# Optimization experiments

Hardware: AMD Instinct MI355X
Metric: run time of the kernel (lower is better)

Reference implementation:

```python
import jax, jax.numpy as jnp
import numpy as np
import math

B, C, N, L = 32, 128, 2048, 1
H, DK, APT = 8, 16, 10
EPS = 1e-5


def conv1x1(x, W, b):
    # 1x1 Conv2d on [B, C, N, L]
    return jnp.einsum('oc,bcnl->bonl', W, x) + b[None, :, None, None]


def layer_norm_12(x):
    # normalize over dims (1, 2) as in the custom LayerNorm (no affine)
    mean = x.mean(axis=(1, 2), keepdims=True)
    var = x.var(axis=(1, 2), keepdims=True)
    return (x - mean) / jnp.sqrt(var + EPS)


def setup_inputs() -> dict:
    key = jax.random.key(0)
    ks = jax.random.split(key, 10)
    s = 0.05  # small-scale init for numerical stability
    inp = {
        'input': jax.random.normal(ks[0], (B, C, N, L), jnp.float32),
        'Wq': jax.random.normal(ks[1], (C, C), jnp.float32) * s,
        'bq': jnp.zeros((C,), jnp.float32),
        'Wv': jax.random.normal(ks[2], (C, C), jnp.float32) * s,
        'bv': jnp.zeros((C,), jnp.float32),
        'Wc': jax.random.normal(ks[3], (C, C), jnp.float32) * s,
        'bc': jnp.zeros((C,), jnp.float32),
        'memory': jax.random.normal(ks[4], (H, L, N, DK), jnp.float32) * s,
        'sa_weight': jnp.ones((C, N, L), jnp.float32),
        'sa_bias': jnp.zeros((C, N, L), jnp.float32),
        'nodevec1': jax.random.normal(ks[5], (N, APT), jnp.float32),
        'nodevec2': jax.random.normal(ks[6], (APT, N), jnp.float32),
        'Wg1': jax.random.normal(ks[7], (C, C), jnp.float32) * s,
        'bg1': jnp.zeros((C,), jnp.float32),
        'Wg2': jax.random.normal(ks[8], (C, C), jnp.float32) * s,
        'bg2': jnp.zeros((C,), jnp.float32),
        'Wg3': jax.random.normal(ks[9], (C, C), jnp.float32) * s,
        'bg3': jnp.zeros((C,), jnp.float32),
    }
    return inp


def reference(input, Wq, bq, Wv, bv, Wc, bc, memory, sa_weight, sa_bias,
              nodevec1, nodevec2, Wg1, bg1, Wg2, bg2, Wg3, bg3):
    scale = math.sqrt(DK)

    def split_heads(t):  # [B,C,N,L] -> [B,H,L,N,DK]
        return t.reshape(B, H, DK, N, L).transpose(0, 1, 4, 3, 2)

    # SpatialAttention (Conv = 1x1 conv + relu; dropout off in eval)
    q = jax.nn.relu(conv1x1(input, Wq, bq))
    v = jax.nn.relu(conv1x1(input, Wv, bv))
    query = jax.nn.softmax(split_heads(q) / scale, axis=-1)     # [B,H,L,N,DK]
    value = split_heads(v)                                       # [B,H,L,N,DK]
    key = jax.nn.softmax(memory / scale, axis=-1)                # [H,L,N,DK]
    Aapt = jax.nn.softmax(jax.nn.relu(nodevec1 @ nodevec2), axis=-1)  # [N,N]

    kv = jnp.einsum('hlnx,bhlny->bhlxy', key, value)             # [B,H,L,DK,DK]
    attn_qkv = jnp.einsum('bhlnx,bhlxy->bhlny', query, kv)       # [B,H,L,N,DK]
    attn_dyn = jnp.einsum('nm,bhlnc->bhlnc', Aapt, value)        # row-sum scaling
    x = attn_qkv + attn_dyn

    # merge heads back to [B,C,N,L] and apply concat conv (Conv = conv+relu)
    x = x.transpose(0, 1, 4, 3, 2).reshape(B, C, N, L)
    x = jax.nn.relu(conv1x1(x, Wc, bc))
    x = x * sa_weight[None] + sa_bias[None] + x                  # affine branch

    # Encoder wrap
    x = x + input
    x = layer_norm_12(x)
    g = conv1x1(x, Wg1, bg1) * jax.nn.sigmoid(conv1x1(x, Wg2, bg2))
    g = conv1x1(g, Wg3, bg3)                                     # GLU
    x = g + x
    x = x * sa_weight[None] + sa_bias[None] + x
    x = layer_norm_12(x)
    return x
```

## Files before the change

kernel.cpp:

```cpp
#include <hip/hip_runtime.h>
#include <math.h>

#define DI __device__ __forceinline__

typedef short bf16x8 __attribute__((ext_vector_type(8)));
typedef float f32x4 __attribute__((ext_vector_type(4)));

constexpr int BB = 32, CC = 128, NN = 2048, HH = 8;
constexpr float EPSf = 1e-5f;
constexpr float RCN = 1.0f / (CC * (float)NN);

#define MFMA(a,b,c) __builtin_amdgcn_mfma_f32_16x16x32_bf16(a,b,c,0,0,0)

DI unsigned short f2b(float f){
    union { float f; unsigned u; } v; v.f = f;
    return (unsigned short)((v.u + 0x7FFFu + ((v.u >> 16) & 1u)) >> 16);
}
DI float b2f(unsigned short h){
    union { unsigned u; float f; } v; v.u = ((unsigned)h) << 16;
    return v.f;
}
DI float sigm(float x){ return 1.0f / (1.0f + __expf(-x)); }

__global__ __launch_bounds__(256) void k_keysm(const float* __restrict__ mem,
                                               unsigned short* __restrict__ ksT)
{
    const int row = blockIdx.x * 256 + threadIdx.x;
    const int h = row >> 11, n = row & 2047;
    const float* p = mem + (size_t)row * 16;
    float v[16];
    f32x4 t0 = *(const f32x4*)(p);
    f32x4 t1 = *(const f32x4*)(p + 4);
    f32x4 t2 = *(const f32x4*)(p + 8);
    f32x4 t3 = *(const f32x4*)(p + 12);
#pragma unroll
    for (int j = 0; j < 4; j++) { v[j] = t0[j]; v[4+j] = t1[j]; v[8+j] = t2[j]; v[12+j] = t3[j]; }
    float mx = v[0];
#pragma unroll
    for (int x = 1; x < 16; x++) mx = fmaxf(mx, v[x]);
    float s = 0.f;
#pragma unroll
    for (int x = 0; x < 16; x++) { v[x] = __expf((v[x] - mx) * 0.25f); s += v[x]; }
    const float is = 1.0f / s;
#pragma unroll
    for (int x = 0; x < 16; x++)
        ksT[((size_t)(h * 16 + x)) * NN + n] = f2b(v[x] * is);
}

__global__ __launch_bounds__(256,2) void k_qv(
    const float* __restrict__ in, const float* __restrict__ Wq, const float* __restrict__ bq,
    const float* __restrict__ Wv, const float* __restrict__ bv,
    unsigned short* __restrict__ qT, unsigned short* __restrict__ vT)
{
    __shared__ unsigned short Wa[128*136];
    __shared__ unsigned short Wb[128*136];
    const int b = blockIdx.x >> 4;
    const int n0 = (blockIdx.x & 15) * 128;
    const int tid = threadIdx.x;
#pragma unroll
    for (int r = 0; r < 16; r++) {
        const int i4 = r * 256 + tid, o = i4 >> 5, cq = i4 & 31;
        f32x4 w1 = *(const f32x4*)&Wq[o*128 + cq*4];
        f32x4 w2 = *(const f32x4*)&Wv[o*128 + cq*4];
        ushort4 p1, p2;
        p1.x=f2b(w1[0]); p1.y=f2b(w1[1]); p1.z=f2b(w1[2]); p1.w=f2b(w1[3]);
        p2.x=f2b(w2[0]); p2.y=f2b(w2[1]); p2.z=f2b(w2[2]); p2.w=f2b(w2[3]);
        *(ushort4*)&Wa[o*136 + cq*4] = p1;
        *(ushort4*)&Wb[o*136 + cq*4] = p2;
    }
    __syncthreads();
    const int l = tid & 63, wid = tid >> 6;
    const int wo = wid & 1, wn = wid >> 1;
    const int lr = l & 15, lg = l >> 4;
    f32x4 accq[4][4], accv[4][4];
    const f32x4 z = {0.f,0.f,0.f,0.f};
#pragma unroll
    for (int i = 0; i < 4; i++)
#pragma unroll
        for (int j = 0; j < 4; j++) { accq[i][j] = z; accv[i][j] = z; }
    const float* inb = in + (size_t)b * CC * NN;
#pragma unroll
    for (int ks = 0; ks < 4; ks++) {
        const int cb = ks*32 + lg*8;
        bf16x8 aq[4], av[4];
#pragma unroll
        for (int mf = 0; mf < 4; mf++) {
            const int o = wo*64 + mf*16 + lr;
            aq[mf] = *(const bf16x8*)&Wa[o*136 + cb];
            av[mf] = *(const bf16x8*)&Wb[o*136 + cb];
        }
        bf16x8 bx[4];
#pragma unroll
        for (int nf = 0; nf < 4; nf++) {
            const int n = n0 + wn*64 + nf*16 + lr;
            union { bf16x8 v; unsigned short u[8]; } t;
#pragma unroll
            for (int j = 0; j < 8; j++) t.u[j] = f2b(inb[(size_t)(cb + j) * NN + n]);
            bx[nf] = t.v;
        }
#pragma unroll
        for (int mf = 0; mf < 4; mf++)
#pragma unroll
            for (int nf = 0; nf < 4; nf++) {
                accq[mf][nf] = MFMA(aq[mf], bx[nf], accq[mf][nf]);
                accv[mf][nf] = MFMA(av[mf], bx[nf], accv[mf][nf]);
            }
    }
#pragma unroll
    for (int mf = 0; mf < 4; mf++) {
        const int ob = wo*64 + mf*16 + lg*4;
        const f32x4 bq4 = *(const f32x4*)&bq[ob];
        const f32x4 bv4 = *(const f32x4*)&bv[ob];
#pragma unroll
        for (int nf = 0; nf < 4; nf++) {
            const int n = n0 + wn*64 + nf*16 + lr;
            const size_t yo = ((size_t)b * NN + n) * CC + ob;
            f32x4 aq_ = accq[mf][nf], av_ = accv[mf][nf];
            ushort4 pq, pv;
            pq.x = f2b(fmaxf(aq_[0]+bq4[0],0.f)); pq.y = f2b(fmaxf(aq_[1]+bq4[1],0.f));
            pq.z = f2b(fmaxf(aq_[2]+bq4[2],0.f)); pq.w = f2b(fmaxf(aq_[3]+bq4[3],0.f));
            pv.x = f2b(fmaxf(av_[0]+bv4[0],0.f)); pv.y = f2b(fmaxf(av_[1]+bv4[1],0.f));
            pv.z = f2b(fmaxf(av_[2]+bv4[2],0.f)); pv.w = f2b(fmaxf(av_[3]+bv4[3],0.f));
            *(ushort4*)&qT[yo] = pq;
            *(ushort4*)&vT[yo] = pv;
        }
    }
}

__global__ __launch_bounds__(256) void k_kv(const unsigned short* __restrict__ ksT,
                                            const unsigned short* __restrict__ vT,
                                            float* __restrict__ kvb)
{
    __shared__ unsigned short vt[4 * 16 * 520];
    const int bh = blockIdx.x;
    const int b = bh >> 3, h = bh & 7;
    const int tid = threadIdx.x, l = tid & 63, wid = tid >> 6;
    const int n0 = wid * 512;
    unsigned short* vtw = vt + wid * (16 * 520);
    const unsigned short* vb = vT + ((size_t)b * NN + n0) * CC + h * 16;
#pragma unroll
    for (int r = 0; r < 8; r++) {
        const int nl = r * 64 + l;
        ushort4 p0 = *(const ushort4*)&vb[(size_t)nl * CC + 0];
        ushort4 p1 = *(const ushort4*)&vb[(size_t)nl * CC + 4];
        ushort4 p2 = *(const ushort4*)&vb[(size_t)nl * CC + 8];
        ushort4 p3 = *(const ushort4*)&vb[(size_t)nl * CC + 12];
        vtw[ 0*520+nl]=p0.x; vtw[ 1*520+nl]=p0.y; vtw[ 2*520+nl]=p0.z; vtw[ 3*520+nl]=p0.w;
        vtw[ 4*520+nl]=p1.x; vtw[ 5*520+nl]=p1.y; vtw[ 6*520+nl]=p1.z; vtw[ 7*520+nl]=p1.w;
        vtw[ 8*520+nl]=p2.x; vtw[ 9*520+nl]=p2.y; vtw[10*520+nl]=p2.z; vtw[11*520+nl]=p2.w;
        vtw[12*520+nl]=p3.x; vtw[13*520+nl]=p3.y; vtw[14*520+nl]=p3.z; vtw[15*520+nl]=p3.w;
    }
    const int lr = l & 15, lg = l >> 4;
    const unsigned short* ka = ksT + (size_t)h * 16 * NN;
    f32x4 acc = {0.f,0.f,0.f,0.f};
#pragma unroll
    for (int kk = 0; kk < 16; kk++) {
        bf16x8 af = *(const bf16x8*)&ka[(size_t)lr * NN + n0 + kk*32 + lg*8];
        bf16x8 bf = *(const bf16x8*)&vtw[lr * 520 + kk*32 + lg*8];
        acc = MFMA(af, bf, acc);
    }
    float* kp = kvb + ((size_t)(b * 8 + h)) * 256;
#pragma unroll
    for (int r = 0; r < 4; r++)
        atomicAdd(&kp[(lg*4 + r) * 16 + lr], acc[r]);
}

__global__ __launch_bounds__(256) void k_attn(unsigned short* __restrict__ qT,
                                              const unsigned short* __restrict__ vT,
                                              const float* __restrict__ kvb)
{
    __shared__ float kvl[8 * 260];
    const int b = blockIdx.x >> 6, nb = blockIdx.x & 63;
    const int tid = threadIdx.x;
    {
        const float* kp = kvb + (size_t)b * 2048 + (tid >> 5) * 256 + (tid & 31) * 8;
        f32x4 v0 = *(const f32x4*)kp;
        f32x4 v1 = *(const f32x4*)(kp + 4);
        float* dst = &kvl[(tid >> 5) * 260 + (tid & 31) * 8];
        *(f32x4*)dst = v0; *(f32x4*)(dst + 4) = v1;
    }
    __syncthreads();
    const int h = tid & 7, nl = tid >> 3;
    const int n = nb * 32 + nl;
    unsigned short* qp = qT + ((size_t)b * NN + n) * CC + h * 16;
    const unsigned short* vp = vT + ((size_t)b * NN + n) * CC + h * 16;
    float q[16];
    {
        uint4 u0 = *(const uint4*)qp, u1 = *(const uint4*)(qp + 8);
        unsigned uu[8] = {u0.x,u0.y,u0.z,u0.w,u1.x,u1.y,u1.z,u1.w};
#pragma unroll
        for (int j = 0; j < 8; j++) {
            q[2*j]   = b2f((unsigned short)(uu[j] & 0xffffu));
            q[2*j+1] = b2f((unsigned short)(uu[j] >> 16));
        }
    }
    float mx = q[0];
#pragma unroll
    for (int x = 1; x < 16; x++) mx = fmaxf(mx, q[x]);
    float p[16]; float s = 0.f;
#pragma unroll
    for (int x = 0; x < 16; x++) { p[x] = __expf((q[x] - mx) * 0.25f); s += p[x]; }
    const float is = 1.0f / s;
    const float* kh = &kvl[h * 260];
    float r[16];
#pragma unroll
    for (int y = 0; y < 16; y++) r[y] = 0.f;
#pragma unroll
    for (int x = 0; x < 16; x++) {
        const float px = p[x];
#pragma unroll
        for (int y = 0; y < 16; y++) r[y] = fmaf(px, kh[x * 16 + y], r[y]);
    }
    unsigned w[8];
    {
        uint4 u0 = *(const uint4*)vp, u1 = *(const uint4*)(vp + 8);
        unsigned uu[8] = {u0.x,u0.y,u0.z,u0.w,u1.x,u1.y,u1.z,u1.w};
#pragma unroll
        for (int j = 0; j < 8; j++) {
            float o0 = r[2*j]   * is + b2f((unsigned short)(uu[j] & 0xffffu));
            float o1 = r[2*j+1] * is + b2f((unsigned short)(uu[j] >> 16));
            w[j] = (unsigned)f2b(o0) | ((unsigned)f2b(o1) << 16);
        }
    }
    uint4 o0; o0.x=w[0]; o0.y=w[1]; o0.z=w[2]; o0.w=w[3];
    uint4 o1; o1.x=w[4]; o1.y=w[5]; o1.z=w[6]; o1.w=w[7];
    *(uint4*)qp = o0; *(uint4*)(qp + 8) = o1;
}

template<int EPI>
__global__ __launch_bounds__(256,2) void k_gemmC(
    const unsigned short* __restrict__ act, const float* __restrict__ W,
    const float* __restrict__ bias, const float* __restrict__ saw,
    const float* __restrict__ sab, const float* __restrict__ in0f,
    const unsigned short* __restrict__ e0b, const float* __restrict__ statsIn,
    float* __restrict__ statsOut, unsigned short* __restrict__ Y)
{
    __shared__ unsigned short Wl[128*136];
    __shared__ float red[8];
    const int b = blockIdx.x >> 4;
    const int n0 = (blockIdx.x & 15) * 128;
    const int tid = threadIdx.x;
    float mean = 0.f, inv = 0.f;
    if (EPI == 1) {
        mean = statsIn[2*b] * RCN;
        const float var = statsIn[2*b+1] * RCN - mean * mean;
        inv = rsqrtf(var + EPSf);
    }
#pragma unroll
    for (int r = 0; r < 16; r++) {
        const int i4 = r * 256 + tid, o = i4 >> 5, cq = i4 & 31;
        f32x4 w1 = *(const f32x4*)&W[o*128 + cq*4];
        ushort4 p1;
        p1.x=f2b(w1[0]); p1.y=f2b(w1[1]); p1.z=f2b(w1[2]); p1.w=f2b(w1[3]);
        *(ushort4*)&Wl[o*136 + cq*4] = p1;
    }
    __syncthreads();
    const int l = tid & 63, wid = tid >> 6;
    const int wo = wid & 1, wn = wid >> 1;
    const int lr = l & 15, lg = l >> 4;
    f32x4 acc[4][4];
    const f32x4 z = {0.f,0.f,0.f,0.f};
#pragma unroll
    for (int i = 0; i < 4; i++)
#pragma unroll
        for (int j = 0; j < 4; j++) acc[i][j] = z;
    const unsigned short* ab = act + (size_t)b * NN * CC;
#pragma unroll
    for (int ks = 0; ks < 4; ks++) {
        const int cb = ks*32 + lg*8;
        bf16x8 af[4];
#pragma unroll
        for (int mf = 0; mf < 4; mf++)
            af[mf] = *(const bf16x8*)&Wl[(wo*64 + mf*16 + lr)*136 + cb];
        bf16x8 bx[4];
#pragma unroll
        for (int nf = 0; nf < 4; nf++)
            bx[nf] = *(const bf16x8*)&ab[(size_t)(n0 + wn*64 + nf*16 + lr) * CC + cb];
#pragma unroll
        for (int mf = 0; mf < 4; mf++)
#pragma unroll
            for (int nf = 0; nf < 4; nf++)
                acc[mf][nf] = MFMA(af[mf], bx[nf], acc[mf][nf]);
    }
    float sum = 0.f, ssq = 0.f;
#pragma unroll
    for (int mf = 0; mf < 4; mf++) {
        const int ob = wo*64 + mf*16 + lg*4;
        const f32x4 b4 = *(const f32x4*)&bias[ob];
#pragma unroll
        for (int nf = 0; nf < 4; nf++) {
            const int n = n0 + wn*64 + nf*16 + lr;
            const size_t yo = ((size_t)b * NN + n) * CC + ob;
            f32x4 a = acc[mf][nf];
            ushort4 eu;
            if (EPI == 1) eu = *(const ushort4*)&e0b[yo];
            ushort4 pk;
            float ys[4];
#pragma unroll
            for (int r = 0; r < 4; r++) {
                const int o = ob + r;
                float t;
                if (EPI == 0) {
                    t = fmaxf(a[r] + b4[r], 0.f);
                } else {
                    const unsigned short ev = (r==0)?eu.x:(r==1)?eu.y:(r==2)?eu.z:eu.w;
                    t = a[r] + b4[r] + (b2f(ev) - mean) * inv;
                }
                const float sw = saw[(size_t)o * NN + n];
                const float sb = sab[(size_t)o * NN + n];
                float y = t * sw + sb + t;
                if (EPI == 0) y += in0f[((size_t)b * CC + o) * NN + n];
                sum += y; ssq += y * y;
                ys[r] = y;
            }
            pk.x = f2b(ys[0]); pk.y = f2b(ys[1]); pk.z = f2b(ys[2]); pk.w = f2b(ys[3]);
            *(ushort4*)&Y[yo] = pk;
        }
    }
#pragma unroll
    for (int off = 32; off > 0; off >>= 1) {
        sum += __shfl_down(sum, off);
        ssq += __shfl_down(ssq, off);
    }
    if ((tid & 63) == 0) { red[wid*2] = sum; red[wid*2+1] = ssq; }
    __syncthreads();
    if (tid == 0) {
        float s = red[0]+red[2]+red[4]+red[6];
        float q = red[1]+red[3]+red[5]+red[7];
        atomicAdd(&statsOut[2*b], s);
        atomicAdd(&statsOut[2*b+1], q);
    }
}

__global__ __launch_bounds__(256,2) void k_glu12(
    const unsigned short* __restrict__ y1, const float* __restrict__ W1,
    const float* __restrict__ b1, const float* __restrict__ W2,
    const float* __restrict__ b2, const float* __restrict__ stats1,
    unsigned short* __restrict__ G)
{
    __shared__ unsigned short Wl1[128*136];
    __shared__ unsigned short Wl2[128*136];
    __shared__ float cs[256];
    const int b = blockIdx.x >> 4;
    const int n0 = (blockIdx.x & 15) * 128;
    const int tid = threadIdx.x;
    const float mean = stats1[2*b] * RCN;
    const float var = stats1[2*b+1] * RCN - mean * mean;
    const float inv = rsqrtf(var + EPSf);
#pragma unroll
    for (int r = 0; r < 16; r++) {
        const int i4 = r * 256 + tid, o = i4 >> 5, cq = i4 & 31;
        f32x4 w1 = *(const f32x4*)&W1[o*128 + cq*4];
        f32x4 w2 = *(const f32x4*)&W2[o*128 + cq*4];
        ushort4 p1, p2;
        p1.x=f2b(w1[0]); p1.y=f2b(w1[1]); p1.z=f2b(w1[2]); p1.w=f2b(w1[3]);
        p2.x=f2b(w2[0]); p2.y=f2b(w2[1]); p2.z=f2b(w2[2]); p2.w=f2b(w2[3]);
        *(ushort4*)&Wl1[o*136 + cq*4] = p1;
        *(ushort4*)&Wl2[o*136 + cq*4] = p2;
    }
    {
        const int o = tid >> 1, hf = tid & 1;
        float s1 = 0.f, s2 = 0.f;
#pragma unroll
        for (int j4 = 0; j4 < 16; j4++) {
            f32x4 a = *(const f32x4*)&W1[o*128 + hf*64 + j4*4];
            f32x4 c = *(const f32x4*)&W2[o*128 + hf*64 + j4*4];
            s1 += a[0]+a[1]+a[2]+a[3];
            s2 += c[0]+c[1]+c[2]+c[3];
        }
        s1 += __shfl_xor(s1, 1);
        s2 += __shfl_xor(s2, 1);
        cs[o]       = b1[o] - mean * inv * s1;
        cs[128 + o] = b2[o] - mean * inv * s2;
    }
    __syncthreads();
    const int l = tid & 63, wid = tid >> 6;
    const int wo = wid & 1, wn = wid >> 1;
    const int lr = l & 15, lg = l >> 4;
    f32x4 acc1[4][4], acc2[4][4];
    const f32x4 z = {0.f,0.f,0.f,0.f};
#pragma unroll
    for (int i = 0; i < 4; i++)
#pragma unroll
        for (int j = 0; j < 4; j++) { acc1[i][j] = z; acc2[i][j] = z; }
    const unsigned short* ab = y1 + (size_t)b * NN * CC;
#pragma unroll
    for (int ks = 0; ks < 4; ks++) {
        const int cb = ks*32 + lg*8;
        bf16x8 a1[4], a2[4];
#pragma unroll
        for (int mf = 0; mf < 4; mf++) {
            const int o = wo*64 + mf*16 + lr;
            a1[mf] = *(const bf16x8*)&Wl1[o*136 + cb];
            a2[mf] = *(const bf16x8*)&Wl2[o*136 + cb];
        }
        bf16x8 bx[4];
#pragma unroll
        for (int nf = 0; nf < 4; nf++)
            bx[nf] = *(const bf16x8*)&ab[(size_t)(n0 + wn*64 + nf*16 + lr) * CC + cb];
#pragma unroll
        for (int mf = 0; mf < 4; mf++)
#pragma unroll
            for (int nf = 0; nf < 4; nf++) {
                acc1[mf][nf] = MFMA(a1[mf], bx[nf], acc1[mf][nf]);
                acc2[mf][nf] = MFMA(a2[mf], bx[nf], acc2[mf][nf]);
            }
    }
#pragma unroll
    for (int mf = 0; mf < 4; mf++) {
        const int ob = wo*64 + mf*16 + lg*4;
        const f32x4 c1 = *(const f32x4*)&cs[ob];
        const f32x4 c2 = *(const f32x4*)&cs[128 + ob];
#pragma unroll
        for (int nf = 0; nf < 4; nf++) {
            const int n = n0 + wn*64 + nf*16 + lr;
            const size_t yo = ((size_t)b * NN + n) * CC + ob;
            ushort4 pk;
            float g1, g2;
            g1 = acc1[mf][nf][0]*inv + c1[0]; g2 = acc2[mf][nf][0]*inv + c2[0];
            pk.x = f2b(g1 * sigm(g2));
            g1 = acc1[mf][nf][1]*inv + c1[1]; g2 = acc2[mf][nf][1]*inv + c2[1];
            pk.y = f2b(g1 * sigm(g2));
            g1 = acc1[mf][nf][2]*inv + c1[2]; g2 = acc2[mf][nf][2]*inv + c2[2];
            pk.z = f2b(g1 * sigm(g2));
            g1 = acc1[mf][nf][3]*inv + c1[3]; g2 = acc2[mf][nf][3]*inv + c2[3];
            pk.w = f2b(g1 * sigm(g2));
            *(ushort4*)&G[yo] = pk;
        }
    }
}

__global__ __launch_bounds__(256) void k_lnfin(const unsigned short* __restrict__ x2,
                                               const float* __restrict__ st,
                                               float* __restrict__ out)
{
    __shared__ unsigned short ts[64*136];
    const int b = blockIdx.x >> 5, n0 = (blockIdx.x & 31) * 64;
    const float mean = st[2*b] * RCN;
    const float var = st[2*b+1] * RCN - mean * mean;
    const float inv = rsqrtf(var + EPSf);
    const int tid = threadIdx.x;
    {
        const int n = tid >> 2, qd = tid & 3;
        const unsigned short* src = x2 + ((size_t)b * NN + n0 + n) * CC + qd * 32;
        uint4 a0 = *(const uint4*)(src);
        uint4 a1 = *(const uint4*)(src + 8);
        uint4 a2 = *(const uint4*)(src + 16);
        uint4 a3 = *(const uint4*)(src + 24);
        unsigned short* d = &ts[n*136 + qd*32];
        *(uint4*)(d) = a0; *(uint4*)(d+8) = a1; *(uint4*)(d+16) = a2; *(uint4*)(d+24) = a3;
    }
    __syncthreads();
    {
        const int c = tid >> 1, nh = tid & 1;
        float* op = out + ((size_t)b * CC + c) * NN + n0 + nh * 32;
        f32x4 buf;
#pragma unroll
        for (int j = 0; j < 32; j++) {
            buf[j & 3] = (b2f(ts[(nh*32 + j)*136 + c]) - mean) * inv;
            if ((j & 3) == 3) *(f32x4*)(op + (j - 3)) = buf;
        }
    }
}

extern "C" void kernel_launch(void* const* d_in, const int* in_sizes, int n_in,
                              void* d_out, int out_size, void* d_ws, size_t ws_size,
                              hipStream_t stream)
{
    const float* input = (const float*)d_in[0];
    const float* Wq  = (const float*)d_in[1];
    const float* bq  = (const float*)d_in[2];
    const float* Wv  = (const float*)d_in[3];
    const float* bv  = (const float*)d_in[4];
    const float* Wc  = (const float*)d_in[5];
    const float* bc  = (const float*)d_in[6];
    const float* mem = (const float*)d_in[7];
    const float* saw = (const float*)d_in[8];
    const float* sab = (const float*)d_in[9];
    const float* Wg1 = (const float*)d_in[12];
    const float* bg1 = (const float*)d_in[13];
    const float* Wg2 = (const float*)d_in[14];
    const float* bg2 = (const float*)d_in[15];
    const float* Wg3 = (const float*)d_in[16];
    const float* bg3 = (const float*)d_in[17];
    float* out = (float*)d_out;

    unsigned char* wsb = (unsigned char*)d_ws;
    unsigned short* qT  = (unsigned short*)(wsb);
    unsigned short* vT  = (unsigned short*)(wsb + 16777216);
    unsigned short* ksT = (unsigned short*)(wsb + 2*16777216);
    float* kvb   = (float*)(wsb + 2*16777216 + 524288);
    float* stats = (float*)(wsb + 2*16777216 + 524288 + 262144);

    hipMemsetAsync(kvb, 0, 262144 + 512, stream);

    k_keysm<<<64,   256, 0, stream>>>(mem, ksT);
    k_qv   <<<512,  256, 0, stream>>>(input, Wq, bq, Wv, bv, qT, vT);
    k_kv   <<<256,  256, 0, stream>>>(ksT, vT, kvb);
    k_attn <<<2048, 256, 0, stream>>>(qT, vT, kvb);
    k_gemmC<0><<<512, 256, 0, stream>>>(qT, Wc, bc, saw, sab, input,
                                        nullptr, nullptr, stats, vT);
    k_glu12<<<512, 256, 0, stream>>>(vT, Wg1, bg1, Wg2, bg2, stats, qT);
    k_gemmC<1><<<512, 256, 0, stream>>>(qT, Wg3, bg3, saw, sab, nullptr,
                                        vT, stats, stats + 64, vT);
    k_lnfin<<<1024, 256, 0, stream>>>(vT, stats + 64, out);
}
```

Before: 143.8 us.

## Fuse attention with concat conv and GLU stages, pre-convert weights once

Adds a prep kernel that converts all six weight matrices to bf16 once and precomputes row sums, so GEMM kernels read bf16 weights straight from global memory instead of converting them into shared memory per block. The attention step is fused with the Wc conv through a shared-memory tile. The three GLU convolutions are fused into one kernel that keeps the intermediate gate tile in LDS. Atomic accumulation for kv and the layer-norm statistics is replaced by per-block partial sums that later kernels reduce, which also removes the memset. The final transpose uses a padded 32-bit shared layout. Trade-offs: higher LDS use per block and repeated partial-sum reductions in each consumer kernel.

Result: faster. 135.4 us (-5.9%).

```diff
diff --git a/kernel.cpp b/kernel.cpp
--- a/kernel.cpp
+++ b/kernel.cpp
@@ -1,4 +1,5 @@
 #include <hip/hip_runtime.h>
+#include <hip/hip_bf16.h>
 #include <math.h>
 
 #define DI __device__ __forceinline__
@@ -6,21 +7,49 @@
 typedef short bf16x8 __attribute__((ext_vector_type(8)));
 typedef float f32x4 __attribute__((ext_vector_type(4)));
 
-constexpr int BB = 32, CC = 128, NN = 2048, HH = 8;
+constexpr int BB = 32, CC = 128, NN = 2048;
 constexpr float EPSf = 1e-5f;
 constexpr float RCN = 1.0f / (CC * (float)NN);
 
 #define MFMA(a,b,c) __builtin_amdgcn_mfma_f32_16x16x32_bf16(a,b,c,0,0,0)
 
 DI unsigned short f2b(float f){
-    union { float f; unsigned u; } v; v.f = f;
-    return (unsigned short)((v.u + 0x7FFFu + ((v.u >> 16) & 1u)) >> 16);
+    union { __hip_bfloat16 h; unsigned short u; } v;
+    v.h = __float2bfloat16(f);
+    return v.u;
 }
 DI float b2f(unsigned short h){
     union { unsigned u; float f; } v; v.u = ((unsigned)h) << 16;
     return v.f;
 }
 DI float sigm(float x){ return 1.0f / (1.0f + __expf(-x)); }
+
+__global__ __launch_bounds__(256) void k_prep(
+    const float* __restrict__ Wq, const float* __restrict__ Wv,
+    const float* __restrict__ Wc, const float* __restrict__ Wg1,
+    const float* __restrict__ Wg2, const float* __restrict__ Wg3,
+    unsigned short* __restrict__ Wb, float* __restrict__ rs)
+{
+    const int tid = threadIdx.x;
+    if (blockIdx.x < 96) {
+        const int i = blockIdx.x * 256 + tid;
+        const int m = i >> 12, q = i & 4095;
+        const float* src = (m==0)?Wq:(m==1)?Wv:(m==2)?Wc:(m==3)?Wg1:(m==4)?Wg2:Wg3;
+        f32x4 w = *(const f32x4*)&src[q * 4];
+        ushort4 p; p.x=f2b(w[0]); p.y=f2b(w[1]); p.z=f2b(w[2]); p.w=f2b(w[3]);
+        *(ushort4*)&Wb[(size_t)m * 16384 + q * 4] = p;
+    } else {
+        const float* src = (tid < 128) ? Wg1 : Wg2;
+        const int o = tid & 127;
+        float s = 0.f;
+#pragma unroll
+        for (int j = 0; j < 32; j++) {
+            f32x4 a = *(const f32x4*)&src[o * 128 + j * 4];
+            s += a[0] + a[1] + a[2] + a[3];
+        }
+        rs[tid] = s;
+    }
+}
 
 __global__ __launch_bounds__(256) void k_keysm(const float* __restrict__ mem,
                                                unsigned short* __restrict__ ksT)
@@ -34,7 +63,7 @@
     f32x4 t2 = *(const f32x4*)(p + 8);
     f32x4 t3 = *(const f32x4*)(p + 12);
 #pragma unroll
-    for (int j = 0; j < 4; j++) { v[j] = t0[j]; v[4+j] = t1[j]; v[8+j] = t2[j]; v[12+j] = t3[j]; }
+    for (int j = 0; j < 4; j++) { v[j]=t0[j]; v[4+j]=t1[j]; v[8+j]=t2[j]; v[12+j]=t3[j]; }
     float mx = v[0];
 #pragma unroll
     for (int x = 1; x < 16; x++) mx = fmaxf(mx, v[x]);
@@ -48,30 +77,14 @@
 }
 
 __global__ __launch_bounds__(256,2) void k_qv(
-    const float* __restrict__ in, const float* __restrict__ Wq, const float* __restrict__ bq,
-    const float* __restrict__ Wv, const float* __restrict__ bv,
-    unsigned short* __restrict__ qT, unsigned short* __restrict__ vT)
-{
-    __shared__ unsigned short Wa[128*136];
-    __shared__ unsigned short Wb[128*136];
-    const int b = blockIdx.x >> 4;
-    const int n0 = (blockIdx.x & 15) * 128;
-    const int tid = threadIdx.x;
-#pragma unroll
-    for (int r = 0; r < 16; r++) {
-        const int i4 = r * 256 + tid, o = i4 >> 5, cq = i4 & 31;
-        f32x4 w1 = *(const f32x4*)&Wq[o*128 + cq*4];
-        f32x4 w2 = *(const f32x4*)&Wv[o*128 + cq*4];
-        ushort4 p1, p2;
-        p1.x=f2b(w1[0]); p1.y=f2b(w1[1]); p1.z=f2b(w1[2]); p1.w=f2b(w1[3]);
-        p2.x=f2b(w2[0]); p2.y=f2b(w2[1]); p2.z=f2b(w2[2]); p2.w=f2b(w2[3]);
-        *(ushort4*)&Wa[o*136 + cq*4] = p1;
-        *(ushort4*)&Wb[o*136 + cq*4] = p2;
-    }
-    __syncthreads();
-    const int l = tid & 63, wid = tid >> 6;
-    const int wo = wid & 1, wn = wid >> 1;
-    const int lr = l & 15, lg = l >> 4;
+    const float* __restrict__ in, const unsigned short* __restrict__ WqB,
+    const unsigned short* __restrict__ WvB, const float* __restrict__ bq,
+    const float* __restrict__ bv, unsigned short* __restrict__ qT,
+    unsigned short* __restrict__ vT)
+{
+    const int b = blockIdx.x >> 4, n0 = (blockIdx.x & 15) * 128;
+    const int tid = threadIdx.x, l = tid & 63, wid = tid >> 6;
+    const int wo = wid & 1, wn = wid >> 1, lr = l & 15, lg = l >> 4;
     f32x4 accq[4][4], accv[4][4];
     const f32x4 z = {0.f,0.f,0.f,0.f};
 #pragma unroll
@@ -81,13 +94,13 @@
     const float* inb = in + (size_t)b * CC * NN;
 #pragma unroll
     for (int ks = 0; ks < 4; ks++) {
-        const int cb = ks*32 + lg*8;
+        const int cb = ks * 32 + lg * 8;
         bf16x8 aq[4], av[4];
 #pragma unroll
         for (int mf = 0; mf < 4; mf++) {
             const int o = wo*64 + mf*16 + lr;
-            aq[mf] = *(const bf16x8*)&Wa[o*136 + cb];
-            av[mf] = *(const bf16x8*)&Wb[o*136 + cb];
+            aq[mf] = *(const bf16x8*)&WqB[o * 128 + cb];
+            av[mf] = *(const bf16x8*)&WvB[o * 128 + cb];
         }
         bf16x8 bx[4];
 #pragma unroll
@@ -132,8 +145,8 @@
                                             float* __restrict__ kvb)
 {
     __shared__ unsigned short vt[4 * 16 * 520];
-    const int bh = blockIdx.x;
-    const int b = bh >> 3, h = bh & 7;
+    __shared__ float red[1024];
+    const int b = blockIdx.x >> 3, h = blockIdx.x & 7;
     const int tid = threadIdx.x, l = tid & 63, wid = tid >> 6;
     const int n0 = wid * 512;
     unsigned short* vtw = vt + wid * (16 * 520);
@@ -159,18 +172,27 @@
         bf16x8 bf = *(const bf16x8*)&vtw[lr * 520 + kk*32 + lg*8];
         acc = MFMA(af, bf, acc);
     }
-    float* kp = kvb + ((size_t)(b * 8 + h)) * 256;
 #pragma unroll
     for (int r = 0; r < 4; r++)
-        atomicAdd(&kp[(lg*4 + r) * 16 + lr], acc[r]);
-}
-
-__global__ __launch_bounds__(256) void k_attn(unsigned short* __restrict__ qT,
-                                              const unsigned short* __restrict__ vT,
-                                              const float* __restrict__ kvb)
+        red[wid * 256 + (lg*4 + r) * 16 + lr] = acc[r];
+    __syncthreads();
+    {
+        const float s = red[tid] + red[256 + tid] + red[512 + tid] + red[768 + tid];
+        kvb[((size_t)(b * 8 + h)) * 256 + tid] = s;
+    }
+}
+
+__global__ __launch_bounds__(256,2) void k_attnC(
+    const unsigned short* __restrict__ qT, unsigned short* __restrict__ vT,
+    const float* __restrict__ kvb, const unsigned short* __restrict__ WcB,
+    const float* __restrict__ bc, const float* __restrict__ saw,
+    const float* __restrict__ sab, const float* __restrict__ in0f,
+    float* __restrict__ part1)
 {
     __shared__ float kvl[8 * 260];
-    const int b = blockIdx.x >> 6, nb = blockIdx.x & 63;
+    __shared__ unsigned short xc[128 * 136];
+    __shared__ float red[8];
+    const int b = blockIdx.x >> 4, n0 = (blockIdx.x & 15) * 128;
     const int tid = threadIdx.x;
     {
         const float* kp = kvb + (size_t)b * 2048 + (tid >> 5) * 256 + (tid & 31) * 8;
@@ -180,102 +202,73 @@
         *(f32x4*)dst = v0; *(f32x4*)(dst + 4) = v1;
     }
     __syncthreads();
-    const int h = tid & 7, nl = tid >> 3;
-    const int n = nb * 32 + nl;
-    unsigned short* qp = qT + ((size_t)b * NN + n) * CC + h * 16;
-    const unsigned short* vp = vT + ((size_t)b * NN + n) * CC + h * 16;
-    float q[16];
-    {
-        uint4 u0 = *(const uint4*)qp, u1 = *(const uint4*)(qp + 8);
-        unsigned uu[8] = {u0.x,u0.y,u0.z,u0.w,u1.x,u1.y,u1.z,u1.w};
-#pragma unroll
-        for (int j = 0; j < 8; j++) {
-            q[2*j]   = b2f((unsigned short)(uu[j] & 0xffffu));
-            q[2*j+1] = b2f((unsigned short)(uu[j] >> 16));
-        }
-    }
-    float mx = q[0];
-#pragma unroll
-    for (int x = 1; x < 16; x++) mx = fmaxf(mx, q[x]);
-    float p[16]; float s = 0.f;
-#pragma unroll
-    for (int x = 0; x < 16; x++) { p[x] = __expf((q[x] - mx) * 0.25f); s += p[x]; }
-    const float is = 1.0f / s;
-    const float* kh = &kvl[h * 260];
-    float r[16];
-#pragma unroll
-    for (int y = 0; y < 16; y++) r[y] = 0.f;
-#pragma unroll
-    for (int x = 0; x < 16; x++) {
-        const float px = p[x];
-#pragma unroll
-        for (int y = 0; y < 16; y++) r[y] = fmaf(px, kh[x * 16 + y], r[y]);
-    }
-    unsigned w[8];
-    {
-        uint4 u0 = *(const uint4*)vp, u1 = *(const uint4*)(vp + 8);
-        unsigned uu[8] = {u0.x,u0.y,u0.z,u0.w,u1.x,u1.y,u1.z,u1.w};
-#pragma unroll
-        for (int j = 0; j < 8; j++) {
-            float o0 = r[2*j]   * is + b2f((unsigned short)(uu[j] & 0xffffu));
-            float o1 = r[2*j+1] * is + b2f((unsigned short)(uu[j] >> 16));
-            w[j] = (unsigned)f2b(o0) | ((unsigned)f2b(o1) << 16);
-        }
-    }
-    uint4 o0; o0.x=w[0]; o0.y=w[1]; o0.z=w[2]; o0.w=w[3];
-    uint4 o1; o1.x=w[4]; o1.y=w[5]; o1.z=w[6]; o1.w=w[7];
-    *(uint4*)qp = o0; *(uint4*)(qp + 8) = o1;
-}
-
-template<int EPI>
-__global__ __launch_bounds__(256,2) void k_gemmC(
-    const unsigned short* __restrict__ act, const float* __restrict__ W,
-    const float* __restrict__ bias, const float* __restrict__ saw,
-    const float* __restrict__ sab, const float* __restrict__ in0f,
-    const unsigned short* __restrict__ e0b, const float* __restrict__ statsIn,
-    float* __restrict__ statsOut, unsigned short* __restrict__ Y)
-{
-    __shared__ unsigned short Wl[128*136];
-    __shared__ float red[8];
-    const int b = blockIdx.x >> 4;
-    const int n0 = (blockIdx.x & 15) * 128;
-    const int tid = threadIdx.x;
-    float mean = 0.f, inv = 0.f;
-    if (EPI == 1) {
-        mean = statsIn[2*b] * RCN;
-        const float var = statsIn[2*b+1] * RCN - mean * mean;
-        inv = rsqrtf(var + EPSf);
-    }
-#pragma unroll
-    for (int r = 0; r < 16; r++) {
-        const int i4 = r * 256 + tid, o = i4 >> 5, cq = i4 & 31;
-        f32x4 w1 = *(const f32x4*)&W[o*128 + cq*4];
-        ushort4 p1;
-        p1.x=f2b(w1[0]); p1.y=f2b(w1[1]); p1.z=f2b(w1[2]); p1.w=f2b(w1[3]);
-        *(ushort4*)&Wl[o*136 + cq*4] = p1;
+#pragma unroll
+    for (int it = 0; it < 4; it++) {
+        const int idx = it * 256 + tid;
+        const int nl = idx >> 3, h = idx & 7;
+        const size_t base = ((size_t)b * NN + n0 + nl) * CC + h * 16;
+        const unsigned short* qp = qT + base;
+        const unsigned short* vp = vT + base;
+        float q[16];
+        {
+            uint4 u0 = *(const uint4*)qp, u1 = *(const uint4*)(qp + 8);
+            unsigned uu[8] = {u0.x,u0.y,u0.z,u0.w,u1.x,u1.y,u1.z,u1.w};
+#pragma unroll
+            for (int j = 0; j < 8; j++) {
+                q[2*j]   = b2f((unsigned short)(uu[j] & 0xffffu));
+                q[2*j+1] = b2f((unsigned short)(uu[j] >> 16));
+            }
+        }
+        float mx = q[0];
+#pragma unroll
+        for (int x = 1; x < 16; x++) mx = fmaxf(mx, q[x]);
+        float p[16]; float s = 0.f;
+#pragma unroll
+        for (int x = 0; x < 16; x++) { p[x] = __expf((q[x] - mx) * 0.25f); s += p[x]; }
+        const float is = 1.0f / s;
+        const float* kh = &kvl[h * 260];
+        float r[16];
+#pragma unroll
+        for (int y = 0; y < 16; y++) r[y] = 0.f;
+#pragma unroll
+        for (int x = 0; x < 16; x++) {
+            const float px = p[x];
+#pragma unroll
+            for (int y = 0; y < 16; y++) r[y] = fmaf(px, kh[x * 16 + y], r[y]);
+        }
+        uint4 w0 = *(const uint4*)vp, w1 = *(const uint4*)(vp + 8);
+        unsigned vv[8] = {w0.x,w0.y,w0.z,w0.w,w1.x,w1.y,w1.z,w1.w};
+        unsigned short* xp = &xc[nl * 136 + h * 16];
+#pragma unroll
+        for (int j2 = 0; j2 < 4; j2++) {
+            ushort4 pk;
+            pk.x = f2b(r[4*j2+0]*is + b2f((unsigned short)(vv[2*j2]   & 0xffffu)));
+            pk.y = f2b(r[4*j2+1]*is + b2f((unsigned short)(vv[2*j2]   >> 16)));
+            pk.z = f2b(r[4*j2+2]*is + b2f((unsigned short)(vv[2*j2+1] & 0xffffu)));
+            pk.w = f2b(r[4*j2+3]*is + b2f((unsigned short)(vv[2*j2+1] >> 16)));
+            *(ushort4*)&xp[j2 * 4] = pk;
+        }
     }
     __syncthreads();
     const int l = tid & 63, wid = tid >> 6;
-    const int wo = wid & 1, wn = wid >> 1;
-    const int lr = l & 15, lg = l >> 4;
+    const int wo = wid & 1, wn = wid >> 1, lr = l & 15, lg = l >> 4;
     f32x4 acc[4][4];
     const f32x4 z = {0.f,0.f,0.f,0.f};
 #pragma unroll
     for (int i = 0; i < 4; i++)
 #pragma unroll
         for (int j = 0; j < 4; j++) acc[i][j] = z;
-    const unsigned short* ab = act + (size_t)b * NN * CC;
 #pragma unroll
     for (int ks = 0; ks < 4; ks++) {
-        const int cb = ks*32 + lg*8;
+        const int cb = ks * 32 + lg * 8;
         bf16x8 af[4];
 #pragma unroll
         for (int mf = 0; mf < 4; mf++)
-            af[mf] = *(const bf16x8*)&Wl[(wo*64 + mf*16 + lr)*136 + cb];
+            af[mf] = *(const bf16x8*)&WcB[(wo*64 + mf*16 + lr) * 128 + cb];
         bf16x8 bx[4];
 #pragma unroll
         for (int nf = 0; nf < 4; nf++)
-            bx[nf] = *(const bf16x8*)&ab[(size_t)(n0 + wn*64 + nf*16 + lr) * CC + cb];
+            bx[nf] = *(const bf16x8*)&xc[(wn*64 + nf*16 + lr) * 136 + cb];
 #pragma unroll
         for (int mf = 0; mf < 4; mf++)
 #pragma unroll
@@ -286,35 +279,26 @@
 #pragma unroll
     for (int mf = 0; mf < 4; mf++) {
         const int ob = wo*64 + mf*16 + lg*4;
-        const f32x4 b4 = *(const f32x4*)&bias[ob];
+        const f32x4 b4 = *(const f32x4*)&bc[ob];
 #pragma unroll
         for (int nf = 0; nf < 4; nf++) {
             const int n = n0 + wn*64 + nf*16 + lr;
             const size_t yo = ((size_t)b * NN + n) * CC + ob;
             f32x4 a = acc[mf][nf];
-            ushort4 eu;
-            if (EPI == 1) eu = *(const ushort4*)&e0b[yo];
-            ushort4 pk;
             float ys[4];
 #pragma unroll
             for (int r = 0; r < 4; r++) {
                 const int o = ob + r;
-                float t;
-                if (EPI == 0) {
-                    t = fmaxf(a[r] + b4[r], 0.f);
-                } else {
-                    const unsigned short ev = (r==0)?eu.x:(r==1)?eu.y:(r==2)?eu.z:eu.w;
-                    t = a[r] + b4[r] + (b2f(ev) - mean) * inv;
-                }
+                const float t = fmaxf(a[r] + b4[r], 0.f);
                 const float sw = saw[(size_t)o * NN + n];
                 const float sb = sab[(size_t)o * NN + n];
-                float y = t * sw + sb + t;
-                if (EPI == 0) y += in0f[((size_t)b * CC + o) * NN + n];
+                float y = t * sw + sb + t + in0f[((size_t)b * CC + o) * NN + n];
                 sum += y; ssq += y * y;
                 ys[r] = y;
             }
+            ushort4 pk;
             pk.x = f2b(ys[0]); pk.y = f2b(ys[1]); pk.z = f2b(ys[2]); pk.w = f2b(ys[3]);
-            *(ushort4*)&Y[yo] = pk;
+            *(ushort4*)&vT[yo] = pk;
         }
     }
 #pragma unroll
@@ -325,121 +309,180 @@
     if ((tid & 63) == 0) { red[wid*2] = sum; red[wid*2+1] = ssq; }
     __syncthreads();
     if (tid == 0) {
-        float s = red[0]+red[2]+red[4]+red[6];
-        float q = red[1]+red[3]+red[5]+red[7];
-        atomicAdd(&statsOut[2*b], s);
-        atomicAdd(&statsOut[2*b+1], q);
-    }
-}
-
-__global__ __launch_bounds__(256,2) void k_glu12(
-    const unsigned short* __restrict__ y1, const float* __restrict__ W1,
-    const float* __restrict__ b1, const float* __restrict__ W2,
-    const float* __restrict__ b2, const float* __restrict__ stats1,
-    unsigned short* __restrict__ G)
-{
-    __shared__ unsigned short Wl1[128*136];
-    __shared__ unsigned short Wl2[128*136];
+        part1[2 * blockIdx.x]     = red[0]+red[2]+red[4]+red[6];
+        part1[2 * blockIdx.x + 1] = red[1]+red[3]+red[5]+red[7];
+    }
+}
+
+__global__ __launch_bounds__(256,2) void k_glu3(
+    const unsigned short* __restrict__ y1,
+    const unsigned short* __restrict__ W1B, const unsigned short* __restrict__ W2B,
+    const unsigned short* __restrict__ W3B,
+    const float* __restrict__ b1, const float* __restrict__ b2,
+    const float* __restrict__ b3, const float* __restrict__ rs,
+    const float* __restrict__ part1, const float* __restrict__ saw,
+    const float* __restrict__ sab, unsigned short* __restrict__ X2,
+    float* __restrict__ part2)
+{
+    __shared__ unsigned short yt[128 * 136];
+    __shared__ unsigned short gx[128 * 136];
     __shared__ float cs[256];
-    const int b = blockIdx.x >> 4;
-    const int n0 = (blockIdx.x & 15) * 128;
+    __shared__ float red[8];
+    const int b = blockIdx.x >> 4, n0 = (blockIdx.x & 15) * 128;
     const int tid = threadIdx.x;
-    const float mean = stats1[2*b] * RCN;
-    const float var = stats1[2*b+1] * RCN - mean * mean;
-    const float inv = rsqrtf(var + EPSf);
-#pragma unroll
-    for (int r = 0; r < 16; r++) {
-        const int i4 = r * 256 + tid, o = i4 >> 5, cq = i4 & 31;
-        f32x4 w1 = *(const f32x4*)&W1[o*128 + cq*4];
-        f32x4 w2 = *(const f32x4*)&W2[o*128 + cq*4];
-        ushort4 p1, p2;
-        p1.x=f2b(w1[0]); p1.y=f2b(w1[1]); p1.z=f2b(w1[2]); p1.w=f2b(w1[3]);
-        p2.x=f2b(w2[0]); p2.y=f2b(w2[1]); p2.z=f2b(w2[2]); p2.w=f2b(w2[3]);
-        *(ushort4*)&Wl1[o*136 + cq*4] = p1;
-        *(ushort4*)&Wl2[o*136 + cq*4] = p2;
-    }
+    float s0 = 0.f, q0 = 0.f;
+#pragma unroll
+    for (int t = 0; t < 16; t++) { s0 += part1[(b*16+t)*2]; q0 += part1[(b*16+t)*2+1]; }
+    const float mean = s0 * RCN;
+    const float var  = q0 * RCN - mean * mean;
+    const float inv  = rsqrtf(var + EPSf);
     {
-        const int o = tid >> 1, hf = tid & 1;
-        float s1 = 0.f, s2 = 0.f;
-#pragma unroll
-        for (int j4 = 0; j4 < 16; j4++) {
-            f32x4 a = *(const f32x4*)&W1[o*128 + hf*64 + j4*4];
-            f32x4 c = *(const f32x4*)&W2[o*128 + hf*64 + j4*4];
-            s1 += a[0]+a[1]+a[2]+a[3];
-            s2 += c[0]+c[1]+c[2]+c[3];
-        }
-        s1 += __shfl_xor(s1, 1);
-        s2 += __shfl_xor(s2, 1);
-        cs[o]       = b1[o] - mean * inv * s1;
-        cs[128 + o] = b2[o] - mean * inv * s2;
+        const int cq = tid & 15;
+#pragma unroll
+        for (int it = 0; it < 8; it++) {
+            const int n = it * 16 + (tid >> 4);
+            uint4 u = *(const uint4*)&y1[((size_t)b * NN + n0 + n) * CC + cq * 8];
+            *(uint4*)&yt[n * 136 + cq * 8] = u;
+        }
+    }
+    {
+        const int o = tid & 127;
+        const float bb = (tid < 128) ? b1[o] : b2[o];
+        cs[tid] = bb - mean * inv * rs[tid];
     }
     __syncthreads();
     const int l = tid & 63, wid = tid >> 6;
-    const int wo = wid & 1, wn = wid >> 1;
-    const int lr = l & 15, lg = l >> 4;
-    f32x4 acc1[4][4], acc2[4][4];
+    const int wo = wid & 1, wn = wid >> 1, lr = l & 15, lg = l >> 4;
+    {
+        f32x4 acc1[4][4], acc2[4][4];
+        const f32x4 z = {0.f,0.f,0.f,0.f};
+#pragma unroll
+        for (int i = 0; i < 4; i++)
+#pragma unroll
+            for (int j = 0; j < 4; j++) { acc1[i][j] = z; acc2[i][j] = z; }
+#pragma unroll
+        for (int ks = 0; ks < 4; ks++) {
+            const int cb = ks * 32 + lg * 8;
+            bf16x8 a1[4], a2[4];
+#pragma unroll
+            for (int mf = 0; mf < 4; mf++) {
+                const int o = wo*64 + mf*16 + lr;
+                a1[mf] = *(const bf16x8*)&W1B[o * 128 + cb];
+                a2[mf] = *(const bf16x8*)&W2B[o * 128 + cb];
+            }
+            bf16x8 bx[4];
+#pragma unroll
+            for (int nf = 0; nf < 4; nf++)
+                bx[nf] = *(const bf16x8*)&yt[(wn*64 + nf*16 + lr) * 136 + cb];
+#pragma unroll
+            for (int mf = 0; mf < 4; mf++)
+#pragma unroll
+                for (int nf = 0; nf < 4; nf++) {
+                    acc1[mf][nf] = MFMA(a1[mf], bx[nf], acc1[mf][nf]);
+                    acc2[mf][nf] = MFMA(a2[mf], bx[nf], acc2[mf][nf]);
+                }
+        }
+#pragma unroll
+        for (int mf = 0; mf < 4; mf++) {
+            const int ob = wo*64 + mf*16 + lg*4;
+            const f32x4 c1 = *(const f32x4*)&cs[ob];
+            const f32x4 c2 = *(const f32x4*)&cs[128 + ob];
+#pragma unroll
+            for (int nf = 0; nf < 4; nf++) {
+                const int nl = wn*64 + nf*16 + lr;
+                ushort4 pk;
+                float g1, g2;
+                g1 = acc1[mf][nf][0]*inv + c1[0]; g2 = acc2[mf][nf][0]*inv + c2[0];
+                pk.x = f2b(g1 * sigm(g2));
+                g1 = acc1[mf][nf][1]*inv + c1[1]; g2 = acc2[mf][nf][1]*inv + c2[1];
+                pk.y = f2b(g1 * sigm(g2));
+                g1 = acc1[mf][nf][2]*inv + c1[2]; g2 = acc2[mf][nf][2]*inv + c2[2];
+                pk.z = f2b(g1 * sigm(g2));
+                g1 = acc1[mf][nf][3]*inv + c1[3]; g2 = acc2[mf][nf][3]*inv + c2[3];
+                pk.w = f2b(g1 * sigm(g2));
+                *(ushort4*)&gx[nl * 136 + ob] = pk;
+            }
+        }
+    }
+    __syncthreads();
+    f32x4 acc[4][4];
     const f32x4 z = {0.f,0.f,0.f,0.f};
 #pragma unroll
     for (int i = 0; i < 4; i++)
 #pragma unroll
-        for (int j = 0; j < 4; j++) { acc1[i][j] = z; acc2[i][j] = z; }
-    const unsigned short* ab = y1 + (size_t)b * NN * CC;
+        for (int j = 0; j < 4; j++) acc[i][j] = z;
 #pragma unroll
     for (int ks = 0; ks < 4; ks++) {
-        const int cb = ks*32 + lg*8;
-        bf16x8 a1[4], a2[4];
-#pragma unroll
-        for (int mf = 0; mf < 4; mf++) {
-            const int o = wo*64 + mf*16 + lr;
-            a1[mf] = *(const bf16x8*)&Wl1[o*136 + cb];
-            a2[mf] = *(const bf16x8*)&Wl2[o*136 + cb];
-        }
+        const int cb = ks * 32 + lg * 8;
+        bf16x8 af[4];
+#pragma unroll
+        for (int mf = 0; mf < 4; mf++)
+            af[mf] = *(const bf16x8*)&W3B[(wo*64 + mf*16 + lr) * 128 + cb];
         bf16x8 bx[4];
 #pragma unroll
         for (int nf = 0; nf < 4; nf++)
-            bx[nf] = *(const bf16x8*)&ab[(size_t)(n0 + wn*64 + nf*16 + lr) * CC + cb];
+            bx[nf] = *(const bf16x8*)&gx[(wn*64 + nf*16 + lr) * 136 + cb];
 #pragma unroll
         for (int mf = 0; mf < 4; mf++)
 #pragma unroll
-            for (int nf = 0; nf < 4; nf++) {
-                acc1[mf][nf] = MFMA(a1[mf], bx[nf], acc1[mf][nf]);
-                acc2[mf][nf] = MFMA(a2[mf], bx[nf], acc2[mf][nf]);
-            }
-    }
+            for (int nf = 0; nf < 4; nf++)
+                acc[mf][nf] = MFMA(af[mf], bx[nf], acc[mf][nf]);
+    }
+    float sum = 0.f, ssq = 0.f;
 #pragma unroll
     for (int mf = 0; mf < 4; mf++) {
         const int ob = wo*64 + mf*16 + lg*4;
-        const f32x4 c1 = *(const f32x4*)&cs[ob];
-        const f32x4 c2 = *(const f32x4*)&cs[128 + ob];
+        const f32x4 b4 = *(const f32x4*)&b3[ob];
 #pragma unroll
         for (int nf = 0; nf < 4; nf++) {
-            const int n = n0 + wn*64 + nf*16 + lr;
+            const int nl = wn*64 + nf*16 + lr;
+            const int n = n0 + nl;
             const size_t yo = ((size_t)b * NN + n) * CC + ob;
+            ushort4 yq = *(const ushort4*)&yt[nl * 136 + ob];
+            f32x4 a = acc[mf][nf];
+            float ys[4];
+#pragma unroll
+            for (int r = 0; r < 4; r++) {
+                const int o = ob + r;
+                const unsigned short ev = (r==0)?yq.x:(r==1)?yq.y:(r==2)?yq.z:yq.w;
+                const float t = a[r] + b4[r] + (b2f(ev) - mean) * inv;
+                const float sw = saw[(size_t)o * NN + n];
+                const float sb = sab[(size_t)o * NN + n];
+                const float y = t * sw + sb + t;
+                sum += y; ssq += y * y;
+                ys[r] = y;
+            }
             ushort4 pk;
-            float g1, g2;
-            g1 = acc1[mf][nf][0]*inv + c1[0]; g2 = acc2[mf][nf][0]*inv + c2[0];
-            pk.x = f2b(g1 * sigm(g2));
-            g1 = acc1[mf][nf][1]*inv + c1[1]; g2 = acc2[mf][nf][1]*inv + c2[1];
-            pk.y = f2b(g1 * sigm(g2));
-            g1 = acc1[mf][nf][2]*inv + c1[2]; g2 = acc2[mf][nf][2]*inv + c2[2];
-            pk.z = f2b(g1 * sigm(g2));
-            g1 = acc1[mf][nf][3]*inv + c1[3]; g2 = acc2[mf][nf][3]*inv + c2[3];
-            pk.w = f2b(g1 * sigm(g2));
-            *(ushort4*)&G[yo] = pk;
-        }
+            pk.x = f2b(ys[0]); pk.y = f2b(ys[1]); pk.z = f2b(ys[2]); pk.w = f2b(ys[3]);
+            *(ushort4*)&X2[yo] = pk;
+        }
+    }
+#pragma unroll
+    for (int off = 32; off > 0; off >>= 1) {
+        sum += __shfl_down(sum, off);
+        ssq += __shfl_down(ssq, off);
+    }
+    if ((tid & 63) == 0) { red[wid*2] = sum; red[wid*2+1] = ssq; }
+    __syncthreads();
+    if (tid == 0) {
+        part2[2 * blockIdx.x]     = red[0]+red[2]+red[4]+red[6];
+        part2[2 * blockIdx.x + 1] = red[1]+red[3]+red[5]+red[7];
     }
 }
 
 __global__ __launch_bounds__(256) void k_lnfin(const unsigned short* __restrict__ x2,
-                                               const float* __restrict__ st,
+                                               const float* __restrict__ part2,
                                                float* __restrict__ out)
 {
-    __shared__ unsigned short ts[64*136];
+    __shared__ unsigned ts[64 * 69];
     const int b = blockIdx.x >> 5, n0 = (blockIdx.x & 31) * 64;
-    const float mean = st[2*b] * RCN;
-    const float var = st[2*b+1] * RCN - mean * mean;
-    const float inv = rsqrtf(var + EPSf);
     const int tid = threadIdx.x;
+    float s0 = 0.f, q0 = 0.f;
+#pragma unroll
+    for (int t = 0; t < 16; t++) { s0 += part2[(b*16+t)*2]; q0 += part2[(b*16+t)*2+1]; }
+    const float mean = s0 * RCN;
+    const float var  = q0 * RCN - mean * mean;
+    const float inv  = rsqrtf(var + EPSf);
     {
         const int n = tid >> 2, qd = tid & 3;
         const unsigned short* src = x2 + ((size_t)b * NN + n0 + n) * CC + qd * 32;
@@ -447,19 +490,26 @@
         uint4 a1 = *(const uint4*)(src + 8);
         uint4 a2 = *(const uint4*)(src + 16);
         uint4 a3 = *(const uint4*)(src + 24);
-        unsigned short* d = &ts[n*136 + qd*32];
-        *(uint4*)(d) = a0; *(uint4*)(d+8) = a1; *(uint4*)(d+16) = a2; *(uint4*)(d+24) = a3;
-    }
-    __syncthreads();
-    {
-        const int c = tid >> 1, nh = tid & 1;
-        float* op = out + ((size_t)b * CC + c) * NN + n0 + nh * 32;
-        f32x4 buf;
-#pragma unroll
-        for (int j = 0; j < 32; j++) {
-            buf[j & 3] = (b2f(ts[(nh*32 + j)*136 + c]) - mean) * inv;
-            if ((j & 3) == 3) *(f32x4*)(op + (j - 3)) = buf;
-        }
+        unsigned u[16] = {a0.x,a0.y,a0.z,a0.w, a1.x,a1.y,a1.z,a1.w,
+                          a2.x,a2.y,a2.z,a2.w, a3.x,a3.y,a3.z,a3.w};
+#pragma unroll
+        for (int k = 0; k < 16; k++)
+            ts[(qd * 16 + k) * 69 + n] = u[k];
+    }
+    __syncthreads();
+#pragma unroll
+    for (int pass = 0; pass < 8; pass++) {
+        const int c = pass * 16 + (tid >> 4), nq = tid & 15;
+        const int cp = c >> 1, hi = c & 1;
+        f32x4 v;
+#pragma unroll
+        for (int j = 0; j < 4; j++) {
+            const unsigned u = ts[cp * 69 + nq * 4 + j];
+            const unsigned short hv = hi ? (unsigned short)(u >> 16)
+                                         : (unsigned short)(u & 0xffffu);
+            v[j] = (b2f(hv) - mean) * inv;
+        }
+        *(f32x4*)&out[((size_t)b * CC + c) * NN + n0 + nq * 4] = v;
     }
 }
 
@@ -488,20 +538,20 @@
     unsigned char* wsb = (unsigned char*)d_ws;
     unsigned short* qT  = (unsigned short*)(wsb);
     unsigned short* vT  = (unsigned short*)(wsb + 16777216);
-    unsigned short* ksT = (unsigned short*)(wsb + 2*16777216);
-    float* kvb   = (float*)(wsb + 2*16777216 + 524288);
-    float* stats = (float*)(wsb + 2*16777216 + 524288 + 262144);
-
-    hipMemsetAsync(kvb, 0, 262144 + 512, stream);
-
+    unsigned short* ksT = (unsigned short*)(wsb + 33554432);
+    float* kvb   = (float*)(wsb + 34078720);
+    unsigned short* Wb  = (unsigned short*)(wsb + 34340864);
+    float* rs    = (float*)(wsb + 34537472);
+    float* part1 = (float*)(wsb + 34538496);
+    float* part2 = (float*)(wsb + 34542592);
+
+    k_prep <<<97,   256, 0, stream>>>(Wq, Wv, Wc, Wg1, Wg2, Wg3, Wb, rs);
     k_keysm<<<64,   256, 0, stream>>>(mem, ksT);
-    k_qv   <<<512,  256, 0, stream>>>(input, Wq, bq, Wv, bv, qT, vT);
+    k_qv   <<<512,  256, 0, stream>>>(input, Wb, Wb + 16384, bq, bv, qT, vT);
     k_kv   <<<256,  256, 0, stream>>>(ksT, vT, kvb);
-    k_attn <<<2048, 256, 0, stream>>>(qT, vT, kvb);
-    k_gemmC<0><<<512, 256, 0, stream>>>(qT, Wc, bc, saw, sab, input,
-                                        nullptr, nullptr, stats, vT);
-    k_glu12<<<512, 256, 0, stream>>>(vT, Wg1, bg1, Wg2, bg2, stats, qT);
-    k_gemmC<1><<<512, 256, 0, stream>>>(qT, Wg3, bg3, saw, sab, nullptr,
-                                        vT, stats, stats + 64, vT);
-    k_lnfin<<<1024, 256, 0, stream>>>(vT, stats + 64, out);
-}
+    k_attnC<<<512,  256, 0, stream>>>(qT, vT, kvb, Wb + 2*16384, bc, saw, sab,
+                                      input, part1);
+    k_glu3 <<<512,  256, 0, stream>>>(vT, Wb + 3*16384, Wb + 4*16384, Wb + 5*16384,
+                                      bg1, bg2, bg3, rs, part1, saw, sab, qT, part2);
+    k_lnfin<<<1024, 256, 0, stream>>>(qT, part2, out);
+}
```
